# Kernel optimization log

Hardware: AMD Instinct MI355X
Metric: run time of the kernel (lower is better)

The kernel has to match this reference:

```python
import jax, jax.numpy as jnp
import numpy as np

NUM_CODES = 4096
EMBED_DIM = 256
N_TOKENS = 65536
COMMITMENT_COST = 0.1


def setup_inputs() -> dict:
    key = jax.random.key(0)
    k1, k2 = jax.random.split(key)
    z_e = jax.random.normal(k1, (N_TOKENS, EMBED_DIM), dtype=jnp.float32)
    embeddings = jax.random.normal(k2, (NUM_CODES, EMBED_DIM), dtype=jnp.float32)
    return {"z_e": z_e, "embeddings": embeddings}


def reference(z_e, embeddings):
    # Squared Euclidean distances (argmin-equivalent to torch.cdist):
    # d2[n,k] = |z_n|^2 - 2 z_n.E_k + |E_k|^2
    z_sq = jnp.sum(z_e * z_e, axis=-1, keepdims=True)          # [N,1]
    e_sq = jnp.sum(embeddings * embeddings, axis=-1)            # [K]
    d2 = z_sq - 2.0 * (z_e @ embeddings.T) + e_sq[None, :]      # [N,K]
    indices = jnp.argmin(d2, axis=-1)                           # [N] int

    z_q = embeddings[indices]                                   # [N,D] gather

    # commitment loss: mse(detach(z_q), z_e)
    diff = jax.lax.stop_gradient(z_q) - z_e
    commitment_loss = COMMITMENT_COST * jnp.mean(diff * diff)

    # straight-through estimator
    z_q_st = z_e + jax.lax.stop_gradient(z_q - z_e)

    # perplexity from code usage histogram (avoids materializing one-hot)
    counts = jnp.zeros((NUM_CODES,), dtype=jnp.float32).at[indices].add(1.0)
    avg_probs = counts / z_e.shape[0]
    perplexity = jnp.exp(-jnp.sum(avg_probs * jnp.log(avg_probs + 1e-10)))

    return z_q_st, indices, commitment_loss, perplexity
```

## Files before the change

kernel.cpp:

```cpp
#include <hip/hip_runtime.h>

#define N_TOKENS   65536
#define NUM_CODES  4096
#define EMBED_DIM  256

#define IDX_OFF  ((size_t)N_TOKENS * EMBED_DIM)
#define LOSS_OFF (IDX_OFF + N_TOKENS)

#define DELTA 0.2f
#define UCAP  16384
#define RT    8

typedef _Float16 half8 __attribute__((ext_vector_type(8)));
typedef float    f32x4 __attribute__((ext_vector_type(4)));
typedef unsigned long long u64;

__device__ __forceinline__ void gl_lds16(const void* g, void* l) {
    __builtin_amdgcn_global_load_lds(
        (const __attribute__((address_space(1))) unsigned int*)g,
        (__attribute__((address_space(3))) unsigned int*)l, 16, 0, 0);
}

__global__ void k_convE(const float* __restrict__ E, _Float16* __restrict__ Eh) {
    int gid = blockIdx.x * 256 + threadIdx.x;
    int n  = gid >> 5;
    int kg = gid & 31;
    const float* src = E + (size_t)n * EMBED_DIM + kg * 8;
    float4 a = *(const float4*)src;
    float4 b = *(const float4*)(src + 4);
    int ct = n >> 4, l15 = n & 15, kc = kg >> 2, q = kg & 3;
    int lane = q * 16 + l15;
    half8 hv;
    hv[0]=(_Float16)a.x; hv[1]=(_Float16)a.y; hv[2]=(_Float16)a.z; hv[3]=(_Float16)a.w;
    hv[4]=(_Float16)b.x; hv[5]=(_Float16)b.y; hv[6]=(_Float16)b.z; hv[7]=(_Float16)b.w;
    *(half8*)(Eh + ((size_t)(ct * 8 + kc) * 64 + lane) * 8) = hv;
}

__global__ void k_esq(const float* __restrict__ E, float* __restrict__ esq) {
    int k = blockIdx.x;
    int l = threadIdx.x;
    float4 v = *(const float4*)(E + (size_t)k * EMBED_DIM + l * 4);
    float s = v.x * v.x + v.y * v.y + v.z * v.z + v.w * v.w;
    #pragma unroll
    for (int off = 32; off; off >>= 1) s += __shfl_down(s, off, 64);
    if (l == 0) esq[k] = s;
}

__global__ void k_transpose(const float* __restrict__ E, float* __restrict__ Et) {
    __shared__ float t[32][33];
    int tx = threadIdx.x & 31, ty = threadIdx.x >> 5;
    int c0 = blockIdx.x * 32, d0 = blockIdx.y * 32;
    #pragma unroll
    for (int i = 0; i < 4; ++i)
        t[ty + 8 * i][tx] = E[(size_t)(c0 + ty + 8 * i) * EMBED_DIM + d0 + tx];
    __syncthreads();
    #pragma unroll
    for (int i = 0; i < 4; ++i)
        Et[(size_t)(d0 + ty + 8 * i) * NUM_CODES + c0 + tx] = t[tx][ty + 8 * i];
}

__launch_bounds__(256, 2)
__global__ void k_argmin_mfma(const float* __restrict__ Z, const _Float16* __restrict__ Eh,
                              const float* __restrict__ esq, int* __restrict__ out_idx,
                              int* __restrict__ ulist, int* __restrict__ ucount) {
    __shared__ __align__(16) _Float16 Bs[16384];
    __shared__ float esq_s[NUM_CODES];

    const int tid  = threadIdx.x;
    const int lane = tid & 63;
    const int w    = tid >> 6;
    const int w0   = w >> 1;
    const int w1   = w & 1;
    const int l15  = lane & 15;
    const int q    = lane >> 4;
    const int tb   = blockIdx.x;

    for (int i = tid; i < NUM_CODES; i += 256) esq_s[i] = esq[i];

    half8 A[4][8];
    const float* Zb = Z + ((size_t)tb * 128 + w0 * 64) * EMBED_DIM;
    #pragma unroll
    for (int rt = 0; rt < 4; ++rt) {
        const float* Zr = Zb + (rt * 16 + l15) * EMBED_DIM + q * 8;
        #pragma unroll
        for (int kc = 0; kc < 8; ++kc) {
            float4 a = *(const float4*)(Zr + kc * 32);
            float4 b = *(const float4*)(Zr + kc * 32 + 4);
            half8 hv;
            hv[0]=(_Float16)a.x; hv[1]=(_Float16)a.y; hv[2]=(_Float16)a.z; hv[3]=(_Float16)a.w;
            hv[4]=(_Float16)b.x; hv[5]=(_Float16)b.y; hv[6]=(_Float16)b.z; hv[7]=(_Float16)b.w;
            A[rt][kc] = hv;
        }
    }

    float best[16], sec[16];
    int   bidx[16];
    #pragma unroll
    for (int k = 0; k < 16; ++k) { best[k] = 1e30f; sec[k] = 1e30f; bidx[k] = 0; }

    const int cb = w1 * 2;

    for (int it = 0; it < NUM_CODES / 64; ++it) {
        __syncthreads();
        const _Float16* src = Eh + (size_t)it * 16384 + (w * 8) * 512 + lane * 8;
        #pragma unroll
        for (int s = 0; s < 8; ++s)
            gl_lds16(src + s * 512, Bs + (w * 8 + s) * 512);
        __syncthreads();

        f32x4 acc[4][2];
        #pragma unroll
        for (int rt = 0; rt < 4; ++rt) { acc[rt][0] = (f32x4)0.0f; acc[rt][1] = (f32x4)0.0f; }

        #pragma unroll
        for (int kc = 0; kc < 8; ++kc) {
            half8 bf0 = *(const half8*)(Bs + ((cb + 0) * 8 + kc) * 512 + lane * 8);
            half8 bf1 = *(const half8*)(Bs + ((cb + 1) * 8 + kc) * 512 + lane * 8);
            #pragma unroll
            for (int rt = 0; rt < 4; ++rt) {
                acc[rt][0] = __builtin_amdgcn_mfma_f32_16x16x32_f16(A[rt][kc], bf0, acc[rt][0], 0, 0, 0);
                acc[rt][1] = __builtin_amdgcn_mfma_f32_16x16x32_f16(A[rt][kc], bf1, acc[rt][1], 0, 0, 0);
            }
        }

        int code0 = it * 64 + cb * 16 + l15;
        #pragma unroll
        for (int c = 0; c < 2; ++c) {
            float e  = esq_s[code0 + c * 16];
            int code = code0 + c * 16;
            #pragma unroll
            for (int rt = 0; rt < 4; ++rt)
                #pragma unroll
                for (int r = 0; r < 4; ++r) {
                    float v = fmaf(-2.0f, acc[rt][c][r], e);
                    int k = rt * 4 + r;
                    float ob = best[k];
                    bool t = v < ob;
                    best[k] = t ? v : ob;
                    sec[k]  = fminf(sec[k], t ? ob : v);
                    bidx[k] = t ? code : bidx[k];
                }
        }
    }

    #pragma unroll
    for (int m = 1; m <= 8; m <<= 1) {
        #pragma unroll
        for (int k = 0; k < 16; ++k) {
            float ob = __shfl_xor(best[k], m, 64);
            float os = __shfl_xor(sec[k],  m, 64);
            int   oi = __shfl_xor(bidx[k], m, 64);
            float ns = fminf(fminf(sec[k], os), fmaxf(best[k], ob));
            bool t = (ob < best[k]) || (ob == best[k] && oi < bidx[k]);
            best[k] = t ? ob : best[k];
            bidx[k] = t ? oi : bidx[k];
            sec[k]  = ns;
        }
    }

    __syncthreads();
    float* mb = (float*)Bs;
    float* ms = mb + 256;
    int*   mi = (int*)(mb + 512);
    if (l15 == 0) {
        #pragma unroll
        for (int k = 0; k < 16; ++k) {
            int row = w0 * 64 + (k >> 2) * 16 + q * 4 + (k & 3);
            mb[row * 2 + w1] = best[k];
            ms[row * 2 + w1] = sec[k];
            mi[row * 2 + w1] = bidx[k];
        }
    }
    __syncthreads();
    if (tid < 128) {
        float b0 = mb[tid * 2], b1 = mb[tid * 2 + 1];
        float s0 = ms[tid * 2], s1 = ms[tid * 2 + 1];
        int   i0 = mi[tid * 2], i1 = mi[tid * 2 + 1];
        bool t = (b1 < b0) || (b1 == b0 && i1 < i0);
        float bb = t ? b1 : b0;
        int   ii = t ? i1 : i0;
        float ss = fminf(fminf(s0, s1), fmaxf(b0, b1));
        int token = tb * 128 + tid;
        out_idx[token] = ii;
        if (ss - bb < DELTA) {
            int p = atomicAdd(ucount, 1);
            if (p < UCAP) ulist[p] = token;
        }
    }
}

__launch_bounds__(256)
__global__ void k_refine(const float* __restrict__ Z, const float* __restrict__ Et,
                         const float* __restrict__ esq, const int* __restrict__ ulist,
                         const int* __restrict__ ucount, u64* __restrict__ umin) {
    int cnt = *ucount; if (cnt > UCAP) cnt = UCAP;
    const int g   = blockIdx.x >> 2;
    const int qtr = blockIdx.x & 3;
    if (g * RT >= cnt) return;

    __shared__ float zs[RT][256];
    const int tid  = threadIdx.x;
    const int lane = tid & 63;

    #pragma unroll
    for (int t = 0; t < RT; ++t) {
        int u = g * RT + t;
        int tok = ulist[(u < cnt) ? u : g * RT];
        zs[t][tid] = Z[(size_t)tok * EMBED_DIM + tid];
    }
    __syncthreads();

    const int c0 = qtr * 1024 + tid * 4;
    f32x4 acc[RT];
    #pragma unroll
    for (int t = 0; t < RT; ++t) acc[t] = (f32x4)0.0f;

    for (int d4 = 0; d4 < 64; ++d4) {
        f32x4 e0 = *(const f32x4*)(Et + (size_t)(d4 * 4 + 0) * NUM_CODES + c0);
        f32x4 e1 = *(const f32x4*)(Et + (size_t)(d4 * 4 + 1) * NUM_CODES + c0);
        f32x4 e2 = *(const f32x4*)(Et + (size_t)(d4 * 4 + 2) * NUM_CODES + c0);
        f32x4 e3 = *(const f32x4*)(Et + (size_t)(d4 * 4 + 3) * NUM_CODES + c0);
        #pragma unroll
        for (int t = 0; t < RT; ++t) {
            f32x4 z4 = *(const f32x4*)&zs[t][d4 * 4];
            acc[t] += z4.x * e0;
            acc[t] += z4.y * e1;
            acc[t] += z4.z * e2;
            acc[t] += z4.w * e3;
        }
    }

    f32x4 eq = *(const f32x4*)(esq + c0);
    #pragma unroll
    for (int t = 0; t < RT; ++t) {
        u64 p = ~0ull;
        #pragma unroll
        for (int r = 0; r < 4; ++r) {
            float v = fmaf(-2.0f, acc[t][r], eq[r]) + 4096.0f;
            u64 cand = ((u64)__float_as_uint(v) << 32) | (unsigned)(c0 + r);
            p = cand < p ? cand : p;
        }
        #pragma unroll
        for (int m = 1; m <= 32; m <<= 1) {
            u64 o = __shfl_xor(p, m, 64);
            p = o < p ? o : p;
        }
        int u = g * RT + t;
        if (lane == 0 && u < cnt) atomicMin(umin + u, p);
    }
}

__global__ void k_rwrite(const int* __restrict__ ulist, const int* __restrict__ ucount,
                         const u64* __restrict__ umin, int* __restrict__ out_idx) {
    int cnt = *ucount; if (cnt > UCAP) cnt = UCAP;
    int u = blockIdx.x * 256 + threadIdx.x;
    if (u < cnt) out_idx[ulist[u]] = (int)(umin[u] & 0xFFFFFFFFu);
}

__global__ void k_gather(const float* __restrict__ Z, const float* __restrict__ E,
                         float* __restrict__ out,
                         float* __restrict__ loss_parts, unsigned* __restrict__ hist) {
    int wave = threadIdx.x >> 6, lane = threadIdx.x & 63;
    int token = blockIdx.x * 4 + wave;
    int* idxi = (int*)(out + IDX_OFF);
    int k = idxi[token];
    float4 z = *(const float4*)(Z + (size_t)token * EMBED_DIM + lane * 4);
    float4 qv = *(const float4*)(E + (size_t)k * EMBED_DIM + lane * 4);
    *(float4*)(out + (size_t)token * EMBED_DIM + lane * 4) = qv;
    float dx = qv.x - z.x, dy = qv.y - z.y, dz = qv.z - z.z, dw = qv.w - z.w;
    float s = dx * dx + dy * dy + dz * dz + dw * dw;
    #pragma unroll
    for (int off = 32; off; off >>= 1) s += __shfl_down(s, off, 64);
    if (lane == 0) {
        atomicAdd(loss_parts + (blockIdx.x & 1023), s);
        atomicAdd(hist + k, 1u);
        out[IDX_OFF + token] = (float)k;
    }
}

__global__ void k_final(const float* __restrict__ loss_parts,
                        const unsigned* __restrict__ hist, float* __restrict__ out) {
    __shared__ float red[256];
    int t = threadIdx.x;
    float s = 0.0f;
    for (int i = t; i < 1024; i += 256) s += loss_parts[i];
    red[t] = s;
    __syncthreads();
    #pragma unroll
    for (int off = 128; off; off >>= 1) {
        if (t < off) red[t] += red[t + off];
        __syncthreads();
    }
    float loss = 0.1f * red[0] / (float)(N_TOKENS * EMBED_DIM);

    float h = 0.0f;
    for (int i = t; i < NUM_CODES; i += 256) {
        float p = (float)hist[i] / (float)N_TOKENS;
        h += p * logf(p + 1e-10f);
    }
    __syncthreads();
    red[t] = h;
    __syncthreads();
    #pragma unroll
    for (int off = 128; off; off >>= 1) {
        if (t < off) red[t] += red[t + off];
        __syncthreads();
    }
    if (t == 0) {
        out[LOSS_OFF]     = loss;
        out[LOSS_OFF + 1] = expf(-red[0]);
    }
}

extern "C" void kernel_launch(void* const* d_in, const int* in_sizes, int n_in,
                              void* d_out, int out_size, void* d_ws, size_t ws_size,
                              hipStream_t stream) {
    const float* Z = (const float*)d_in[0];
    const float* E = (const float*)d_in[1];
    float* out = (float*)d_out;
    char*  ob  = (char*)d_out;
    char*  ws  = (char*)d_ws;

    _Float16* Eh   = (_Float16*)(ob + 50331648);
    float*    Et   = (float*)(ob + 54525952);
    u64*      umin = (u64*)(ob + 58720256);
    int*      idx  = (int*)(out + IDX_OFF);

    float*    esq        = (float*)ws;
    int*      ulist      = (int*)(ws + 16384);
    int*      ucount     = (int*)(ws + 81920);
    float*    loss_parts = (float*)(ws + 81984);
    unsigned* hist       = (unsigned*)(ws + 86080);

    hipMemsetAsync(ws + 81920, 0, 64 + 4096 + 16384, stream);
    hipMemsetAsync(umin, 0xFF, (size_t)UCAP * 8, stream);

    k_convE      <<<(NUM_CODES * 32) / 256, 256, 0, stream>>>(E, Eh);
    k_esq        <<<NUM_CODES, 64, 0, stream>>>(E, esq);
    k_transpose  <<<dim3(NUM_CODES / 32, EMBED_DIM / 32), 256, 0, stream>>>(E, Et);
    k_argmin_mfma<<<N_TOKENS / 128, 256, 0, stream>>>(Z, Eh, esq, idx, ulist, ucount);
    k_refine     <<<4 * (UCAP / RT), 256, 0, stream>>>(Z, Et, esq, ulist, ucount, umin);
    k_rwrite     <<<UCAP / 256, 256, 0, stream>>>(ulist, ucount, umin, idx);
    k_gather     <<<N_TOKENS / 4, 256, 0, stream>>>(Z, E, out, loss_parts, hist);
    k_final      <<<1, 256, 0, stream>>>(loss_parts, hist, out);
}
```

Before: 342.8 us.

## Double-buffer codebook tiles in LDS with async prefetch and manual waitcnt

Splits the shared codebook tile into two buffers and prefetches tile it+2 while computing tile it. Explicit vmcnt waits and raw barriers replace the two __syncthreads per iteration, so global-to-LDS loads overlap the MFMA work. It also raises wave priority around the MFMA block and restructures the argmin update to compare the two code candidates pairwise first. LDS use roughly doubles for the tile and correctness now depends on the hand-written vmcnt counts and barriers, including esq_s being ready before first use.

```diff
diff --git a/kernel.cpp b/kernel.cpp
--- a/kernel.cpp
+++ b/kernel.cpp
@@ -59,11 +59,11 @@
         Et[(size_t)(d0 + ty + 8 * i) * NUM_CODES + c0 + tx] = t[tx][ty + 8 * i];
 }
 
-__launch_bounds__(256, 2)
-__global__ void k_argmin_mfma(const float* __restrict__ Z, const _Float16* __restrict__ Eh,
-                              const float* __restrict__ esq, int* __restrict__ out_idx,
-                              int* __restrict__ ulist, int* __restrict__ ucount) {
-    __shared__ __align__(16) _Float16 Bs[16384];
+__global__ __launch_bounds__(256) __attribute__((amdgpu_waves_per_eu(2, 2)))
+void k_argmin_mfma(const float* __restrict__ Z, const _Float16* __restrict__ Eh,
+                   const float* __restrict__ esq, int* __restrict__ out_idx,
+                   int* __restrict__ ulist, int* __restrict__ ucount) {
+    __shared__ __align__(16) _Float16 Bs[2][16384];
     __shared__ float esq_s[NUM_CODES];
 
     const int tid  = threadIdx.x;
@@ -74,6 +74,18 @@
     const int l15  = lane & 15;
     const int q    = lane >> 4;
     const int tb   = blockIdx.x;
+    const int cb   = w1 * 2;
+
+#define STAGE(itn, bb) do {                                                        \
+        const _Float16* _src = Eh + ((size_t)(itn) << 14) + (w * 8) * 512 + lane * 8; \
+        _Float16* _dst = &Bs[bb][(w * 8) * 512];                                   \
+        _Pragma("unroll")                                                          \
+        for (int s = 0; s < 8; ++s)                                                \
+            gl_lds16(_src + s * 512, _dst + s * 512);                              \
+    } while (0)
+
+    STAGE(0, 0);
+    STAGE(1, 1);
 
     for (int i = tid; i < NUM_CODES; i += 256) esq_s[i] = esq[i];
 
@@ -98,50 +110,58 @@
     #pragma unroll
     for (int k = 0; k < 16; ++k) { best[k] = 1e30f; sec[k] = 1e30f; bidx[k] = 0; }
 
-    const int cb = w1 * 2;
+    __syncthreads();
 
     for (int it = 0; it < NUM_CODES / 64; ++it) {
-        __syncthreads();
-        const _Float16* src = Eh + (size_t)it * 16384 + (w * 8) * 512 + lane * 8;
-        #pragma unroll
-        for (int s = 0; s < 8; ++s)
-            gl_lds16(src + s * 512, Bs + (w * 8 + s) * 512);
-        __syncthreads();
+        const int b = it & 1;
+
+        if (it == NUM_CODES / 64 - 1) asm volatile("s_waitcnt vmcnt(0)" ::: "memory");
+        else                          asm volatile("s_waitcnt vmcnt(8)" ::: "memory");
+        asm volatile("s_barrier" ::: "memory");
 
         f32x4 acc[4][2];
         #pragma unroll
         for (int rt = 0; rt < 4; ++rt) { acc[rt][0] = (f32x4)0.0f; acc[rt][1] = (f32x4)0.0f; }
 
+        __builtin_amdgcn_s_setprio(1);
         #pragma unroll
         for (int kc = 0; kc < 8; ++kc) {
-            half8 bf0 = *(const half8*)(Bs + ((cb + 0) * 8 + kc) * 512 + lane * 8);
-            half8 bf1 = *(const half8*)(Bs + ((cb + 1) * 8 + kc) * 512 + lane * 8);
+            half8 bf0 = *(const half8*)(&Bs[b][((cb + 0) * 8 + kc) * 512 + lane * 8]);
+            half8 bf1 = *(const half8*)(&Bs[b][((cb + 1) * 8 + kc) * 512 + lane * 8]);
             #pragma unroll
             for (int rt = 0; rt < 4; ++rt) {
                 acc[rt][0] = __builtin_amdgcn_mfma_f32_16x16x32_f16(A[rt][kc], bf0, acc[rt][0], 0, 0, 0);
                 acc[rt][1] = __builtin_amdgcn_mfma_f32_16x16x32_f16(A[rt][kc], bf1, acc[rt][1], 0, 0, 0);
             }
         }
-
-        int code0 = it * 64 + cb * 16 + l15;
-        #pragma unroll
-        for (int c = 0; c < 2; ++c) {
-            float e  = esq_s[code0 + c * 16];
-            int code = code0 + c * 16;
+        __builtin_amdgcn_s_setprio(0);
+
+        asm volatile("s_barrier" ::: "memory");
+        if (it + 2 < NUM_CODES / 64) STAGE(it + 2, b);
+
+        const int code0 = it * 64 + cb * 16 + l15;
+        const int code1 = code0 + 16;
+        const float e0 = esq_s[code0];
+        const float e1 = esq_s[code1];
+        #pragma unroll
+        for (int rt = 0; rt < 4; ++rt)
             #pragma unroll
-            for (int rt = 0; rt < 4; ++rt)
-                #pragma unroll
-                for (int r = 0; r < 4; ++r) {
-                    float v = fmaf(-2.0f, acc[rt][c][r], e);
-                    int k = rt * 4 + r;
-                    float ob = best[k];
-                    bool t = v < ob;
-                    best[k] = t ? v : ob;
-                    sec[k]  = fminf(sec[k], t ? ob : v);
-                    bidx[k] = t ? code : bidx[k];
-                }
-        }
-    }
+            for (int r = 0; r < 4; ++r) {
+                int k = rt * 4 + r;
+                float v0 = fmaf(-2.0f, acc[rt][0][r], e0);
+                float v1 = fmaf(-2.0f, acc[rt][1][r], e1);
+                bool pw  = v1 < v0;
+                float wv = pw ? v1 : v0;
+                float lv = pw ? v0 : v1;
+                int   wi = pw ? code1 : code0;
+                float ob = best[k];
+                bool t = wv < ob;
+                sec[k]  = fminf(fminf(fmaxf(ob, wv), lv), sec[k]);
+                best[k] = t ? wv : ob;
+                bidx[k] = t ? wi : bidx[k];
+            }
+    }
+#undef STAGE
 
     #pragma unroll
     for (int m = 1; m <= 8; m <<= 1) {
```

Result: slower. 356.2 us (+3.9%).
